# Performance work log

Measured on AMD Instinct MI355X. Metric: run time of the kernel, lower is better.

Reference implementation:

```python
import jax, jax.numpy as jnp
import numpy as np
import math

B, S, D, H, V = 2, 2048, 512, 4, 32000
WINDOWS = [None, 128, 512, None]  # per-head attention windows (None = unlimited)


def setup_inputs() -> dict:
    key = jax.random.key(0)
    ks = jax.random.split(key, 8)
    input_ids = jax.random.randint(ks[0], (B, S), 0, V, dtype=jnp.int64)
    padding_mask = jnp.zeros((B, S), dtype=bool)  # True = pad
    embed_table = jax.random.normal(ks[1], (V, D), dtype=jnp.float32) * 0.02
    self_factors = jnp.full((H,), 0.1, dtype=jnp.float32)
    distance_alphas = jnp.full((H,), 0.1, dtype=jnp.float32)
    # torch Linear weights: [out_features, in_features], xavier-uniform init
    lim_f = math.sqrt(6.0 / (H * D + D))
    fusion_w = jax.random.uniform(ks[2], (D, H * D), jnp.float32, -lim_f, lim_f)
    fusion_b = jnp.zeros((D,), jnp.float32)
    lim_o = math.sqrt(6.0 / (D + V))
    out_w = jax.random.uniform(ks[3], (V, D), jnp.float32, -lim_o, lim_o)
    out_b = jnp.zeros((V,), jnp.float32)
    return {
        "input_ids": input_ids,
        "padding_mask": padding_mask,
        "embed_table": embed_table,
        "self_factors": self_factors,
        "distance_alphas": distance_alphas,
        "fusion_w": fusion_w,
        "fusion_b": fusion_b,
        "out_w": out_w,
        "out_b": out_b,
    }


def reference(input_ids, padding_mask, embed_table, self_factors,
              distance_alphas, fusion_w, fusion_b, out_w, out_b):
    b, s = input_ids.shape
    d = embed_table.shape[1]
    h = self_factors.shape[0]

    emb = embed_table[input_ids]  # [B,S,D]

    pos = jnp.arange(s)
    dist = jnp.abs(pos[:, None] - pos[None, :])          # [S,S]
    causal = pos[None, :] > pos[:, None]                  # [S,S] strict upper triangle
    eye = dist == 0                                       # [S,S]

    # shared raw scores, computed once (same for all heads)
    base = jnp.einsum('bqd,bkd->bqk', emb, emb) / math.sqrt(d)  # [B,S,S]

    # per-head distance decay bias: [H,S,S]
    decay = 1.0 / (1.0 + distance_alphas[:, None, None] * dist.astype(jnp.float32))

    scores = base[None, :, :, :] * decay[:, None, :, :]   # [H,B,S,S]
    # diagonal self-factor scaling
    scores = jnp.where(eye[None, None],
                       scores * self_factors[:, None, None, None], scores)

    # per-head window mask (None -> window >= S, never masks)
    win = jnp.array([s if w is None else w for w in WINDOWS[:h]])
    window_mask = dist[None, :, :] > win[:, None, None]   # [H,S,S]

    # key padding mask, diagonal exempted (as in original)
    key_pad = padding_mask[:, None, :] & (~eye[None])      # [B,S,S]

    full_mask = (window_mask[:, None] | causal[None, None] | key_pad[None])  # [H,B,S,S]
    scores = jnp.where(full_mask, -jnp.inf, scores)

    attn = jax.nn.softmax(scores, axis=-1)                 # [H,B,S,S]
    ctx = jnp.einsum('hbqk,bkd->hbqd', attn, emb)          # [H,B,S,D]

    concat = jnp.moveaxis(ctx, 0, 2).reshape(b, s, h * d)  # [B,S,H*D]
    fused = concat @ fusion_w.T + fusion_b                 # [B,S,D]
    logits = fused @ out_w.T + out_b                       # [B,S,V]
    return logits
```

## Files before the change

### kernel.cpp

```cpp
#include <hip/hip_runtime.h>
#include <hip/hip_bf16.h>
#include <stdint.h>

#define BB 2
#define SB 2048
#define DD 512
#define HH 4
#define VV 32000

typedef __attribute__((ext_vector_type(4))) float f32x4;
typedef __attribute__((ext_vector_type(8))) short bf16x8;
typedef __attribute__((ext_vector_type(4))) unsigned short us4;

__device__ __forceinline__ unsigned short f2bf(float f) {
    unsigned u = __float_as_uint(f);
    u += 0x7fffu + ((u >> 16) & 1u);
    return (unsigned short)(u >> 16);
}

__device__ __forceinline__ __attribute__((address_space(3))) unsigned int*
as_lds(void* p) {
    return (__attribute__((address_space(3))) unsigned int*)(unsigned)(uintptr_t)p;
}
__device__ __forceinline__ const __attribute__((address_space(1))) unsigned int*
as_gbl(const void* p) {
    return (const __attribute__((address_space(1))) unsigned int*)(uintptr_t)p;
}

__global__ void k_cvt_bf16(const float* __restrict__ src, unsigned short* __restrict__ dst, int n) {
    int idx = (blockIdx.x * blockDim.x + threadIdx.x) * 4;
    int stride = gridDim.x * blockDim.x * 4;
    for (int i = idx; i < n; i += stride) {
        float4 v = *(const float4*)(src + i);
        us4 o;
        o.x = f2bf(v.x); o.y = f2bf(v.y); o.z = f2bf(v.z); o.w = f2bf(v.w);
        *(us4*)(dst + i) = o;
    }
}

__global__ void k_embed(const int* __restrict__ ids, const float* __restrict__ tbl,
                        unsigned short* __restrict__ emb) {
    int row = blockIdx.x;
    int id = ids[row];
    if (id < 0) id = 0;
    if (id >= VV) id = VV - 1;
    const float* s = tbl + (size_t)id * DD;
    unsigned short* d = emb + (size_t)row * DD;
    int t = threadIdx.x;
    d[t]       = f2bf(s[t]);
    d[t + 256] = f2bf(s[t + 256]);
}

__global__ void k_dtab_lsum(const float* __restrict__ als,
                            float* __restrict__ dtab, float* __restrict__ lsum) {
    int i = blockIdx.x * 256 + threadIdx.x;
    if (i < HH * SB) {
        int h = i >> 11, d = i & (SB - 1);
        dtab[i] = 0.04419417382415922f / (1.f + als[h] * (float)d);
    } else {
        lsum[i - HH * SB] = 0.f;
    }
}

__global__ void k_embT(const unsigned short* __restrict__ emb, unsigned short* __restrict__ embT) {
    const int d0 = blockIdx.x * 64, s0 = blockIdx.y * 64, b = blockIdx.z;
    __shared__ unsigned short TT[64][72];
    const int t = threadIdx.x;
    {
        int s = t >> 2, c16 = (t & 3) * 16;
        const unsigned short* src = emb + ((size_t)(b * SB + s0 + s)) * DD + d0 + c16;
        bf16x8 v0 = *(const bf16x8*)src;
        bf16x8 v1 = *(const bf16x8*)(src + 8);
#pragma unroll
        for (int j = 0; j < 8; ++j) {
            TT[c16 + j][s]     = (unsigned short)v0[j];
            TT[c16 + 8 + j][s] = (unsigned short)v1[j];
        }
    }
    __syncthreads();
    {
        int d = t >> 2, sc = (t & 3) * 16;
        bf16x8 o0, o1;
#pragma unroll
        for (int j = 0; j < 8; ++j) {
            o0[j] = (short)TT[d][sc + j];
            o1[j] = (short)TT[d][sc + 8 + j];
        }
        unsigned short* dst = embT + ((size_t)(b * DD + d0 + d)) * SB + s0 + sc;
        *(bf16x8*)dst = o0;
        *(bf16x8*)(dst + 8) = o1;
    }
}

__launch_bounds__(256, 2)
__global__ void k_base(const unsigned short* __restrict__ emb,
                       const unsigned char* __restrict__ pad,
                       const float* __restrict__ sfs,
                       const float* __restrict__ dtab,
                       unsigned short* __restrict__ P,
                       float* __restrict__ lsum)
{
    const int kt = blockIdx.x, qt = blockIdx.y, b = blockIdx.z;
    if (kt > qt + 1) return;
    const int tid = threadIdx.x, lane = tid & 63, wv = tid >> 6;
    const int l15 = lane & 15, g = lane >> 4;

    if (kt == qt + 1) {
        int row = tid >> 2, cb = (tid & 3) * 16;
        int4 z = {0, 0, 0, 0};
#pragma unroll
        for (int h = 0; h < 4; ++h) {
            unsigned short* Ph = P + (((size_t)(h * 2 + b)) * SB + qt * 64 + row) * SB + kt * 64 + cb;
            *(int4*)Ph = z;
            *(int4*)(Ph + 8) = z;
        }
        return;
    }

    __shared__ __align__(16) unsigned short Ql[64 * 128];
    __shared__ __align__(16) unsigned short Kl[64 * 128];

    const int q = qt * 64 + wv * 16 + l15;

    f32x4 zero4 = {0.f, 0.f, 0.f, 0.f};
    f32x4 cc[4];
#pragma unroll
    for (int c = 0; c < 4; ++c) cc[c] = zero4;

    for (int dc = 0; dc < 4; ++dc) {
        const int d0 = dc * 128;
        __syncthreads();
#pragma unroll
        for (int i = 0; i < 4; ++i) {
            int flat = (i * 256 + tid) * 8;
            int row = flat >> 7;
            int ch  = (flat >> 3) & 15;
            int scol = ((ch ^ (row & 15)) << 3);
            __builtin_amdgcn_global_load_lds(
                as_gbl(emb + ((size_t)(b * SB + qt * 64 + row)) * DD + d0 + scol),
                as_lds(Ql + flat), 16, 0, 0);
            __builtin_amdgcn_global_load_lds(
                as_gbl(emb + ((size_t)(b * SB + kt * 64 + row)) * DD + d0 + scol),
                as_lds(Kl + flat), 16, 0, 0);
        }
        asm volatile("s_waitcnt vmcnt(0)" ::: "memory");
        __syncthreads();

#pragma unroll
        for (int dsl = 0; dsl < 4; ++dsl) {
            int chr = (dsl * 4 + g);
            bf16x8 qf = *(const bf16x8*)(Ql + (wv * 16 + l15) * 128 + ((chr ^ l15) << 3));
#pragma unroll
            for (int c = 0; c < 4; ++c) {
                bf16x8 kf = *(const bf16x8*)(Kl + (c * 16 + l15) * 128 + ((chr ^ l15) << 3));
                cc[c] = __builtin_amdgcn_mfma_f32_16x16x32_bf16(kf, qf, cc[c], 0, 0, 0);
            }
        }
    }

    unsigned long long padm = __ballot(pad[(size_t)b * SB + kt * 64 + lane] != 0);

    const int wins[4] = {1 << 30, 128, 512, 1 << 30};
#pragma unroll
    for (int h = 0; h < 4; ++h) {
        const int win = wins[h];
        if (kt * 64 + win + 192 < qt * 64) continue;
        const float sf = sfs[h];
        const float* dth = dtab + h * SB;
        float rsum = 0.f;
        unsigned short pb[4][4];
#pragma unroll
        for (int c = 0; c < 4; ++c) {
#pragma unroll
            for (int r = 0; r < 4; ++r) {
                int kk = kt * 64 + c * 16 + 4 * g + r;
                int dist = q - kk;
                float p = 0.f;
                if (dist >= 0 && dist <= win &&
                    ((dist == 0) || !((padm >> (c * 16 + 4 * g + r)) & 1ull))) {
                    float s = cc[c][r] * dth[dist];
                    if (dist == 0) s *= sf;
                    p = __expf(s);
                }
                rsum += p;
                pb[c][r] = f2bf(p);
            }
        }
        unsigned short* Ph = P + (((size_t)(h * 2 + b)) * SB + q) * SB + kt * 64;
#pragma unroll
        for (int c = 0; c < 4; ++c) {
            us4 o;
            o.x = pb[c][0]; o.y = pb[c][1]; o.z = pb[c][2]; o.w = pb[c][3];
            *(us4*)(Ph + c * 16 + 4 * g) = o;
        }
        rsum += __shfl_xor(rsum, 16, 64);
        rsum += __shfl_xor(rsum, 32, 64);
        if (lane < 16)
            atomicAdd(&lsum[((size_t)(h * 2 + b)) * SB + q], rsum);
    }
}

__launch_bounds__(256, 2)
__global__ void k_pv(const unsigned short* __restrict__ P,
                     const unsigned short* __restrict__ embT,
                     const float* __restrict__ lsum,
                     unsigned short* __restrict__ concat)
{
    const int t64 = blockIdx.x, b = blockIdx.y, h = blockIdx.z;
    const int mt = t64 >> 2, nt = t64 & 3;
    const int Q0 = mt * 128;
    const int win = (h == 1) ? 128 : (h == 2) ? 512 : (1 << 30);
    int klo = Q0 - win - 64; if (klo < 0) klo = 0; klo &= ~63;
    const int khi = Q0 + 128;

    __shared__ __align__(16) unsigned short Al[128 * 32];
    __shared__ __align__(16) unsigned short Bl[128 * 32];

    const int tid = threadIdx.x, lane = tid & 63, wv = tid >> 6;
    const int wm = (wv >> 1) * 64, wn = (wv & 1) * 64;
    const int l15 = lane & 15, g = lane >> 4;

    f32x4 zero4 = {0.f, 0.f, 0.f, 0.f};
    f32x4 acc[4][4];
#pragma unroll
    for (int i = 0; i < 4; ++i)
#pragma unroll
        for (int j = 0; j < 4; ++j) acc[i][j] = zero4;

    const unsigned short* Ab = P + (((size_t)(h * 2 + b)) * SB + Q0) * SB;
    const unsigned short* Bb = embT + ((size_t)(b * DD + nt * 128)) * SB;

    for (int k0 = klo; k0 < khi; k0 += 32) {
        __syncthreads();
#pragma unroll
        for (int s = 0; s < 2; ++s) {
            int e = (s * 256 + tid) * 8;
            int row = e >> 5, col = e & 31;
            __builtin_amdgcn_global_load_lds(as_gbl(Ab + (size_t)row * SB + k0 + col),
                                             as_lds(Al + e), 16, 0, 0);
            __builtin_amdgcn_global_load_lds(as_gbl(Bb + (size_t)row * SB + k0 + col),
                                             as_lds(Bl + e), 16, 0, 0);
        }
        asm volatile("s_waitcnt vmcnt(0)" ::: "memory");
        __syncthreads();

        bf16x8 af[4], bfr[4];
#pragma unroll
        for (int i = 0; i < 4; ++i) {
            af[i]  = *(const bf16x8*)(Al + (wm + i * 16 + l15) * 32 + 8 * g);
            bfr[i] = *(const bf16x8*)(Bl + (wn + i * 16 + l15) * 32 + 8 * g);
        }
#pragma unroll
        for (int i = 0; i < 4; ++i)
#pragma unroll
            for (int j = 0; j < 4; ++j)
                acc[i][j] = __builtin_amdgcn_mfma_f32_16x16x32_bf16(af[i], bfr[j], acc[i][j], 0, 0, 0);
    }

    const float* ls = lsum + ((size_t)(h * 2 + b)) * SB;
    unsigned short* cb = concat + ((size_t)(b * SB)) * (HH * DD) + h * DD + nt * 128;
#pragma unroll
    for (int i = 0; i < 4; ++i) {
        int rowb = wm + i * 16 + g * 4;
        float inv[4];
#pragma unroll
        for (int rr = 0; rr < 4; ++rr) inv[rr] = 1.f / ls[Q0 + rowb + rr];
#pragma unroll
        for (int j = 0; j < 4; ++j) {
            int col = wn + j * 16 + l15;
#pragma unroll
            for (int rr = 0; rr < 4; ++rr)
                cb[(size_t)(Q0 + rowb + rr) * (HH * DD) + col] = f2bf(acc[i][j][rr] * inv[rr]);
        }
    }
}

template <int OUTF32>
__launch_bounds__(256, 2)
__global__ void k_gemm_bt(const unsigned short* __restrict__ A,
                          const unsigned short* __restrict__ Bt,
                          const float* __restrict__ bias,
                          void* __restrict__ Cout,
                          int M, int N, int K)
{
    const int nMt = M >> 7;
    const int nwg = gridDim.x;
    int bid = blockIdx.x;
    int q = nwg >> 3, r = nwg & 7;
    int x = bid & 7, o = bid >> 3;
    int wg = (x < r ? x * (q + 1) : r * (q + 1) + (x - r) * q) + o;
    const int mt = wg % nMt, nt = wg / nMt;

    __shared__ __align__(16) unsigned short Al[128 * 32];
    __shared__ __align__(16) unsigned short Bl[128 * 32];

    const int tid = threadIdx.x;
    const int lane = tid & 63;
    const int wv = tid >> 6;
    const int wm = (wv >> 1) * 64, wn = (wv & 1) * 64;
    const int l15 = lane & 15, g = lane >> 4;

    f32x4 zero4 = {0.f, 0.f, 0.f, 0.f};
    f32x4 acc[4][4];
#pragma unroll
    for (int i = 0; i < 4; ++i)
#pragma unroll
        for (int j = 0; j < 4; ++j) acc[i][j] = zero4;

    const unsigned short* Ab = A + (size_t)mt * 128 * K;
    const unsigned short* Bb = Bt + (size_t)nt * 128 * K;

    for (int k0 = 0; k0 < K; k0 += 32) {
        __syncthreads();
#pragma unroll
        for (int s = 0; s < 2; ++s) {
            int e = (s * 256 + tid) * 8;
            int row = e >> 5, col = e & 31;
            __builtin_amdgcn_global_load_lds(as_gbl(Ab + (size_t)row * K + k0 + col),
                                             as_lds(Al + e), 16, 0, 0);
            __builtin_amdgcn_global_load_lds(as_gbl(Bb + (size_t)row * K + k0 + col),
                                             as_lds(Bl + e), 16, 0, 0);
        }
        asm volatile("s_waitcnt vmcnt(0)" ::: "memory");
        __syncthreads();

        bf16x8 af[4], bfr[4];
#pragma unroll
        for (int i = 0; i < 4; ++i) {
            af[i]  = *(const bf16x8*)(Al + (wm + i * 16 + l15) * 32 + 8 * g);
            bfr[i] = *(const bf16x8*)(Bl + (wn + i * 16 + l15) * 32 + 8 * g);
        }
#pragma unroll
        for (int i = 0; i < 4; ++i)
#pragma unroll
            for (int j = 0; j < 4; ++j)
                acc[i][j] = __builtin_amdgcn_mfma_f32_16x16x32_bf16(af[i], bfr[j], acc[i][j], 0, 0, 0);
    }

#pragma unroll
    for (int i = 0; i < 4; ++i) {
        int rowb = mt * 128 + wm + i * 16 + g * 4;
#pragma unroll
        for (int j = 0; j < 4; ++j) {
            int col = nt * 128 + wn + j * 16 + l15;
            float bv = bias[col];
            if (OUTF32) {
                float* C = (float*)Cout;
#pragma unroll
                for (int rr = 0; rr < 4; ++rr)
                    C[(size_t)(rowb + rr) * N + col] = acc[i][j][rr] + bv;
            } else {
                unsigned short* C = (unsigned short*)Cout;
#pragma unroll
                for (int rr = 0; rr < 4; ++rr)
                    C[(size_t)(rowb + rr) * N + col] = f2bf(acc[i][j][rr] + bv);
            }
        }
    }
}

extern "C" void kernel_launch(void* const* d_in, const int* in_sizes, int n_in,
                              void* d_out, int out_size, void* d_ws, size_t ws_size,
                              hipStream_t stream)
{
    const int*           ids = (const int*)d_in[0];
    const unsigned char* pad = (const unsigned char*)d_in[1];
    const float*         tbl = (const float*)d_in[2];
    const float*         sfs = (const float*)d_in[3];
    const float*         als = (const float*)d_in[4];
    const float*         fw  = (const float*)d_in[5];
    const float*         fb  = (const float*)d_in[6];
    const float*         ow  = (const float*)d_in[7];
    const float*         ob  = (const float*)d_in[8];
    float* logits = (float*)d_out;

    char* ws = (char*)d_ws;
    unsigned short* outw_bf = (unsigned short*)(ws);
    unsigned short* fusw_bf = (unsigned short*)(ws + 32768000);
    unsigned short* emb_bf  = (unsigned short*)(ws + 34865152);
    unsigned short* concat  = (unsigned short*)(ws + 39059456);
    unsigned short* fused   = (unsigned short*)(ws + 55836672);

    char* ob_scratch = (char*)d_out;
    unsigned short* P    = (unsigned short*)(ob_scratch);
    unsigned short* embT = (unsigned short*)(ob_scratch + 67108864);
    float*          dtab = (float*)(ob_scratch + 71303168);
    float*          lsum = (float*)(ob_scratch + 71335936);

    k_cvt_bf16<<<2048, 256, 0, stream>>>(ow, outw_bf, VV * DD);
    k_cvt_bf16<<<512, 256, 0, stream>>>(fw, fusw_bf, DD * HH * DD);
    k_embed<<<BB * SB, 256, 0, stream>>>(ids, tbl, emb_bf);
    k_dtab_lsum<<<96, 256, 0, stream>>>(als, dtab, lsum);

    dim3 tg(8, 32, BB);
    k_embT<<<tg, 256, 0, stream>>>(emb_bf, embT);

    dim3 bg(32, 32, BB);
    k_base<<<bg, 256, 0, stream>>>(emb_bf, pad, sfs, dtab, P, lsum);

    dim3 pg(64, BB, HH);
    k_pv<<<pg, 256, 0, stream>>>(P, embT, lsum, concat);

    k_gemm_bt<0><<<32 * 4, 256, 0, stream>>>(concat, fusw_bf, fb, fused, BB * SB, DD, HH * DD);
    k_gemm_bt<1><<<32 * 250, 256, 0, stream>>>(fused, outw_bf, ob, logits, BB * SB, VV, DD);
}
```

Baseline: 394.8 us.

## Merge prep kernels into one launch and add 256x256 output-projection GEMM

Folds the four preprocessing kernels (weight bf16 conversion, embedding gather, decay table, transpose) into a single block-indexed launch. The transpose now reads the embedding table directly, so it no longer waits on the bf16 embedding buffer. The large vocab projection switches to a new 512-thread GEMM with 256x256 tiles, a 4-deep global_load_lds pipeline, XOR-swizzled LDS, priority hints and XCD-aware block remapping. This cuts launch overhead and raises data reuse in the dominant GEMM, at the cost of higher LDS use (128KB) and register pressure.

```diff
diff --git a/kernel.cpp b/kernel.cpp
--- a/kernel.cpp
+++ b/kernel.cpp
@@ -27,68 +27,87 @@
     return (const __attribute__((address_space(1))) unsigned int*)(uintptr_t)p;
 }
 
-__global__ void k_cvt_bf16(const float* __restrict__ src, unsigned short* __restrict__ dst, int n) {
-    int idx = (blockIdx.x * blockDim.x + threadIdx.x) * 4;
-    int stride = gridDim.x * blockDim.x * 4;
-    for (int i = idx; i < n; i += stride) {
-        float4 v = *(const float4*)(src + i);
-        us4 o;
-        o.x = f2bf(v.x); o.y = f2bf(v.y); o.z = f2bf(v.z); o.w = f2bf(v.w);
-        *(us4*)(dst + i) = o;
-    }
-}
-
-__global__ void k_embed(const int* __restrict__ ids, const float* __restrict__ tbl,
-                        unsigned short* __restrict__ emb) {
-    int row = blockIdx.x;
-    int id = ids[row];
-    if (id < 0) id = 0;
-    if (id >= VV) id = VV - 1;
-    const float* s = tbl + (size_t)id * DD;
-    unsigned short* d = emb + (size_t)row * DD;
-    int t = threadIdx.x;
-    d[t]       = f2bf(s[t]);
-    d[t + 256] = f2bf(s[t + 256]);
-}
-
-__global__ void k_dtab_lsum(const float* __restrict__ als,
-                            float* __restrict__ dtab, float* __restrict__ lsum) {
-    int i = blockIdx.x * 256 + threadIdx.x;
-    if (i < HH * SB) {
-        int h = i >> 11, d = i & (SB - 1);
-        dtab[i] = 0.04419417382415922f / (1.f + als[h] * (float)d);
+__device__ __forceinline__ bf16x8 ldsrd(const unsigned short* base, int row, int g) {
+    int byte = row * 64 + (((g) ^ (row & 3)) << 4);
+    return *(const bf16x8*)((const char*)base + byte);
+}
+
+__global__ void k_prep(const int* __restrict__ ids, const float* __restrict__ tbl,
+                       const float* __restrict__ als,
+                       const float* __restrict__ fw, const float* __restrict__ ow,
+                       unsigned short* __restrict__ outw_bf, unsigned short* __restrict__ fusw_bf,
+                       unsigned short* __restrict__ emb, unsigned short* __restrict__ embT,
+                       float* __restrict__ dtab, float* __restrict__ lsum)
+{
+    __shared__ unsigned short TT[64][72];
+    const int bid = blockIdx.x, t = threadIdx.x;
+
+    if (bid < 2000) {
+        int base = bid * 8192 + t * 4;
+#pragma unroll
+        for (int it = 0; it < 8; ++it) {
+            int i = base + it * 1024;
+            float4 v = *(const float4*)(ow + i);
+            us4 o; o.x = f2bf(v.x); o.y = f2bf(v.y); o.z = f2bf(v.z); o.w = f2bf(v.w);
+            *(us4*)(outw_bf + i) = o;
+        }
+    } else if (bid < 2256) {
+        int base = (bid - 2000) * 4096 + t * 4;
+#pragma unroll
+        for (int it = 0; it < 4; ++it) {
+            int i = base + it * 1024;
+            float4 v = *(const float4*)(fw + i);
+            us4 o; o.x = f2bf(v.x); o.y = f2bf(v.y); o.z = f2bf(v.z); o.w = f2bf(v.w);
+            *(us4*)(fusw_bf + i) = o;
+        }
+    } else if (bid < 6352) {
+        int row = bid - 2256;
+        int id = ids[row];
+        if (id < 0) id = 0;
+        if (id >= VV) id = VV - 1;
+        const float* s = tbl + (size_t)id * DD;
+        unsigned short* d = emb + (size_t)row * DD;
+        d[t]       = f2bf(s[t]);
+        d[t + 256] = f2bf(s[t + 256]);
+    } else if (bid < 6448) {
+        int i = (bid - 6352) * 256 + t;
+        if (i < HH * SB) {
+            int h = i >> 11, dd = i & (SB - 1);
+            dtab[i] = 0.04419417382415922f / (1.f + als[h] * (float)dd);
+        } else {
+            lsum[i - HH * SB] = 0.f;
+        }
     } else {
-        lsum[i - HH * SB] = 0.f;
-    }
-}
-
-__global__ void k_embT(const unsigned short* __restrict__ emb, unsigned short* __restrict__ embT) {
-    const int d0 = blockIdx.x * 64, s0 = blockIdx.y * 64, b = blockIdx.z;
-    __shared__ unsigned short TT[64][72];
-    const int t = threadIdx.x;
-    {
-        int s = t >> 2, c16 = (t & 3) * 16;
-        const unsigned short* src = emb + ((size_t)(b * SB + s0 + s)) * DD + d0 + c16;
-        bf16x8 v0 = *(const bf16x8*)src;
-        bf16x8 v1 = *(const bf16x8*)(src + 8);
-#pragma unroll
-        for (int j = 0; j < 8; ++j) {
-            TT[c16 + j][s]     = (unsigned short)v0[j];
-            TT[c16 + 8 + j][s] = (unsigned short)v1[j];
-        }
-    }
-    __syncthreads();
-    {
-        int d = t >> 2, sc = (t & 3) * 16;
-        bf16x8 o0, o1;
-#pragma unroll
-        for (int j = 0; j < 8; ++j) {
-            o0[j] = (short)TT[d][sc + j];
-            o1[j] = (short)TT[d][sc + 8 + j];
-        }
-        unsigned short* dst = embT + ((size_t)(b * DD + d0 + d)) * SB + s0 + sc;
-        *(bf16x8*)dst = o0;
-        *(bf16x8*)(dst + 8) = o1;
+        int bid2 = bid - 6448;
+        const int d0 = (bid2 & 7) * 64, s0 = ((bid2 >> 3) & 31) * 64, b = bid2 >> 8;
+        {
+            int s = t >> 2, c16 = (t & 3) * 16;
+            int id = ids[b * SB + s0 + s];
+            if (id < 0) id = 0;
+            if (id >= VV) id = VV - 1;
+            const float* src = tbl + (size_t)id * DD + d0 + c16;
+#pragma unroll
+            for (int q4 = 0; q4 < 4; ++q4) {
+                float4 v = *(const float4*)(src + q4 * 4);
+                TT[c16 + q4 * 4 + 0][s] = f2bf(v.x);
+                TT[c16 + q4 * 4 + 1][s] = f2bf(v.y);
+                TT[c16 + q4 * 4 + 2][s] = f2bf(v.z);
+                TT[c16 + q4 * 4 + 3][s] = f2bf(v.w);
+            }
+        }
+        __syncthreads();
+        {
+            int d = t >> 2, sc = (t & 3) * 16;
+            bf16x8 o0, o1;
+#pragma unroll
+            for (int j = 0; j < 8; ++j) {
+                o0[j] = (short)TT[d][sc + j];
+                o1[j] = (short)TT[d][sc + 8 + j];
+            }
+            unsigned short* dst = embT + ((size_t)(b * DD + d0 + d)) * SB + s0 + sc;
+            *(bf16x8*)dst = o0;
+            *(bf16x8*)(dst + 8) = o1;
+        }
     }
 }
 
@@ -359,6 +378,153 @@
     }
 }
 
+__launch_bounds__(512, 2)
+__global__ void k_gemm256(const unsigned short* __restrict__ A,
+                          const unsigned short* __restrict__ Bt,
+                          const float* __restrict__ bias,
+                          float* __restrict__ Cout,
+                          int M, int N, int K)
+{
+    const int nMt = M >> 8;
+    const int nwg = gridDim.x;
+    int bid = blockIdx.x;
+    int q = nwg >> 3, r = nwg & 7;
+    int x = bid & 7, o = bid >> 3;
+    int wg = (x < r ? x * (q + 1) : r * (q + 1) + (x - r) * q) + o;
+    const int mt = wg % nMt, nt = wg / nMt;
+
+    __shared__ __align__(16) unsigned short Al[4][8192];
+    __shared__ __align__(16) unsigned short Bl[4][8192];
+
+    const int tid = threadIdx.x;
+    const int lane = tid & 63, wv = tid >> 6;
+    const int wr = wv >> 2, wc = wv & 3;
+    const int l15 = lane & 15, g = lane >> 4;
+
+    f32x4 zero4 = {0.f, 0.f, 0.f, 0.f};
+    f32x4 acc[8][4];
+#pragma unroll
+    for (int i = 0; i < 8; ++i)
+#pragma unroll
+        for (int j = 0; j < 4; ++j) acc[i][j] = zero4;
+
+    const unsigned short* Ab = A + (size_t)mt * 256 * K;
+    const unsigned short* Bb = Bt + (size_t)nt * 256 * K;
+
+    const int c0 = tid, c1 = 512 + tid;
+    const int r0 = c0 >> 2, r1 = c1 >> 2;
+    const int sc0 = (((c0 & 3) ^ (r0 & 3)) << 3);
+    const int sc1 = (((c1 & 3) ^ (r1 & 3)) << 3);
+    const unsigned short* Asrc0 = Ab + (size_t)r0 * K + sc0;
+    const unsigned short* Asrc1 = Ab + (size_t)r1 * K + sc1;
+    const unsigned short* Bsrc0 = Bb + (size_t)r0 * K + sc0;
+    const unsigned short* Bsrc1 = Bb + (size_t)r1 * K + sc1;
+
+#define STAGE_A256(rg_, ko_) { \
+    __builtin_amdgcn_global_load_lds(as_gbl(Asrc0 + (ko_)), as_lds(&Al[rg_][c0 * 8]), 16, 0, 0); \
+    __builtin_amdgcn_global_load_lds(as_gbl(Asrc1 + (ko_)), as_lds(&Al[rg_][c1 * 8]), 16, 0, 0); }
+#define STAGE_B256(rg_, ko_) { \
+    __builtin_amdgcn_global_load_lds(as_gbl(Bsrc0 + (ko_)), as_lds(&Bl[rg_][c0 * 8]), 16, 0, 0); \
+    __builtin_amdgcn_global_load_lds(as_gbl(Bsrc1 + (ko_)), as_lds(&Bl[rg_][c1 * 8]), 16, 0, 0); }
+
+#define SBAR { __builtin_amdgcn_sched_barrier(0); __builtin_amdgcn_s_barrier(); __builtin_amdgcn_sched_barrier(0); }
+
+#define GEMM_GROUP(t_, DOSTAGE_, WAIT_)                                          \
+  {                                                                              \
+    const int rg = (t_) & 3;                                                     \
+    const unsigned short* Ar = Al[rg];                                           \
+    const unsigned short* Br = Bl[rg];                                           \
+    bf16x8 bfr0 = ldsrd(Br, wc * 64 +  0 + l15, g);                              \
+    bf16x8 bfr1 = ldsrd(Br, wc * 64 + 16 + l15, g);                              \
+    bf16x8 bfr2 = ldsrd(Br, wc * 64 + 32 + l15, g);                              \
+    bf16x8 bfr3 = ldsrd(Br, wc * 64 + 48 + l15, g);                              \
+    bf16x8 af0 = ldsrd(Ar, wr * 128 +  0 + l15, g);                              \
+    bf16x8 af1 = ldsrd(Ar, wr * 128 + 16 + l15, g);                              \
+    bf16x8 af2 = ldsrd(Ar, wr * 128 + 32 + l15, g);                              \
+    bf16x8 af3 = ldsrd(Ar, wr * 128 + 48 + l15, g);                              \
+    if (DOSTAGE_) STAGE_A256(((t_) + 3) & 3, ((t_) + 3) * 32);                   \
+    SBAR;                                                                        \
+    __builtin_amdgcn_s_setprio(1);                                               \
+    acc[0][0] = __builtin_amdgcn_mfma_f32_16x16x32_bf16(af0, bfr0, acc[0][0], 0, 0, 0); \
+    acc[0][1] = __builtin_amdgcn_mfma_f32_16x16x32_bf16(af0, bfr1, acc[0][1], 0, 0, 0); \
+    acc[0][2] = __builtin_amdgcn_mfma_f32_16x16x32_bf16(af0, bfr2, acc[0][2], 0, 0, 0); \
+    acc[0][3] = __builtin_amdgcn_mfma_f32_16x16x32_bf16(af0, bfr3, acc[0][3], 0, 0, 0); \
+    acc[1][0] = __builtin_amdgcn_mfma_f32_16x16x32_bf16(af1, bfr0, acc[1][0], 0, 0, 0); \
+    acc[1][1] = __builtin_amdgcn_mfma_f32_16x16x32_bf16(af1, bfr1, acc[1][1], 0, 0, 0); \
+    acc[1][2] = __builtin_amdgcn_mfma_f32_16x16x32_bf16(af1, bfr2, acc[1][2], 0, 0, 0); \
+    acc[1][3] = __builtin_amdgcn_mfma_f32_16x16x32_bf16(af1, bfr3, acc[1][3], 0, 0, 0); \
+    acc[2][0] = __builtin_amdgcn_mfma_f32_16x16x32_bf16(af2, bfr0, acc[2][0], 0, 0, 0); \
+    acc[2][1] = __builtin_amdgcn_mfma_f32_16x16x32_bf16(af2, bfr1, acc[2][1], 0, 0, 0); \
+    acc[2][2] = __builtin_amdgcn_mfma_f32_16x16x32_bf16(af2, bfr2, acc[2][2], 0, 0, 0); \
+    acc[2][3] = __builtin_amdgcn_mfma_f32_16x16x32_bf16(af2, bfr3, acc[2][3], 0, 0, 0); \
+    acc[3][0] = __builtin_amdgcn_mfma_f32_16x16x32_bf16(af3, bfr0, acc[3][0], 0, 0, 0); \
+    acc[3][1] = __builtin_amdgcn_mfma_f32_16x16x32_bf16(af3, bfr1, acc[3][1], 0, 0, 0); \
+    acc[3][2] = __builtin_amdgcn_mfma_f32_16x16x32_bf16(af3, bfr2, acc[3][2], 0, 0, 0); \
+    acc[3][3] = __builtin_amdgcn_mfma_f32_16x16x32_bf16(af3, bfr3, acc[3][3], 0, 0, 0); \
+    __builtin_amdgcn_s_setprio(0);                                               \
+    SBAR;                                                                        \
+    bf16x8 ag0 = ldsrd(Ar, wr * 128 +  64 + l15, g);                             \
+    bf16x8 ag1 = ldsrd(Ar, wr * 128 +  80 + l15, g);                             \
+    bf16x8 ag2 = ldsrd(Ar, wr * 128 +  96 + l15, g);                             \
+    bf16x8 ag3 = ldsrd(Ar, wr * 128 + 112 + l15, g);                             \
+    if (DOSTAGE_) STAGE_B256(((t_) + 3) & 3, ((t_) + 3) * 32);                   \
+    WAIT_;                                                                       \
+    SBAR;                                                                        \
+    __builtin_amdgcn_s_setprio(1);                                               \
+    acc[4][0] = __builtin_amdgcn_mfma_f32_16x16x32_bf16(ag0, bfr0, acc[4][0], 0, 0, 0); \
+    acc[4][1] = __builtin_amdgcn_mfma_f32_16x16x32_bf16(ag0, bfr1, acc[4][1], 0, 0, 0); \
+    acc[4][2] = __builtin_amdgcn_mfma_f32_16x16x32_bf16(ag0, bfr2, acc[4][2], 0, 0, 0); \
+    acc[4][3] = __builtin_amdgcn_mfma_f32_16x16x32_bf16(ag0, bfr3, acc[4][3], 0, 0, 0); \
+    acc[5][0] = __builtin_amdgcn_mfma_f32_16x16x32_bf16(ag1, bfr0, acc[5][0], 0, 0, 0); \
+    acc[5][1] = __builtin_amdgcn_mfma_f32_16x16x32_bf16(ag1, bfr1, acc[5][1], 0, 0, 0); \
+    acc[5][2] = __builtin_amdgcn_mfma_f32_16x16x32_bf16(ag1, bfr2, acc[5][2], 0, 0, 0); \
+    acc[5][3] = __builtin_amdgcn_mfma_f32_16x16x32_bf16(ag1, bfr3, acc[5][3], 0, 0, 0); \
+    acc[6][0] = __builtin_amdgcn_mfma_f32_16x16x32_bf16(ag2, bfr0, acc[6][0], 0, 0, 0); \
+    acc[6][1] = __builtin_amdgcn_mfma_f32_16x16x32_bf16(ag2, bfr1, acc[6][1], 0, 0, 0); \
+    acc[6][2] = __builtin_amdgcn_mfma_f32_16x16x32_bf16(ag2, bfr2, acc[6][2], 0, 0, 0); \
+    acc[6][3] = __builtin_amdgcn_mfma_f32_16x16x32_bf16(ag2, bfr3, acc[6][3], 0, 0, 0); \
+    acc[7][0] = __builtin_amdgcn_mfma_f32_16x16x32_bf16(ag3, bfr0, acc[7][0], 0, 0, 0); \
+    acc[7][1] = __builtin_amdgcn_mfma_f32_16x16x32_bf16(ag3, bfr1, acc[7][1], 0, 0, 0); \
+    acc[7][2] = __builtin_amdgcn_mfma_f32_16x16x32_bf16(ag3, bfr2, acc[7][2], 0, 0, 0); \
+    acc[7][3] = __builtin_amdgcn_mfma_f32_16x16x32_bf16(ag3, bfr3, acc[7][3], 0, 0, 0); \
+    __builtin_amdgcn_s_setprio(0);                                               \
+    SBAR;                                                                        \
+  }
+
+    const int NT = K >> 5;
+    STAGE_A256(0, 0);  STAGE_B256(0, 0);
+    STAGE_A256(1, 32); STAGE_B256(1, 32);
+    STAGE_A256(2, 64); STAGE_B256(2, 64);
+    asm volatile("s_waitcnt vmcnt(8)" ::: "memory");
+    SBAR;
+
+    for (int t = 0; t < NT - 3; ++t) {
+        GEMM_GROUP(t, 1, asm volatile("s_waitcnt vmcnt(8)" ::: "memory"));
+    }
+    GEMM_GROUP(NT - 3, 0, asm volatile("s_waitcnt vmcnt(4)" ::: "memory"));
+    GEMM_GROUP(NT - 2, 0, asm volatile("s_waitcnt vmcnt(0)" ::: "memory"));
+    GEMM_GROUP(NT - 1, 0, );
+
+    const int mrow = mt * 256 + wr * 128;
+    const int ncol = nt * 256 + wc * 64;
+#pragma unroll
+    for (int i = 0; i < 8; ++i) {
+        int rowb = mrow + i * 16 + g * 4;
+#pragma unroll
+        for (int j = 0; j < 4; ++j) {
+            int col = ncol + j * 16 + l15;
+            float bv = bias[col];
+#pragma unroll
+            for (int rr = 0; rr < 4; ++rr)
+                Cout[(size_t)(rowb + rr) * N + col] = acc[i][j][rr] + bv;
+        }
+    }
+#undef GEMM_GROUP
+#undef STAGE_A256
+#undef STAGE_B256
+#undef SBAR
+}
+
 extern "C" void kernel_launch(void* const* d_in, const int* in_sizes, int n_in,
                               void* d_out, int out_size, void* d_ws, size_t ws_size,
                               hipStream_t stream)
@@ -387,13 +553,8 @@
     float*          dtab = (float*)(ob_scratch + 71303168);
     float*          lsum = (float*)(ob_scratch + 71335936);
 
-    k_cvt_bf16<<<2048, 256, 0, stream>>>(ow, outw_bf, VV * DD);
-    k_cvt_bf16<<<512, 256, 0, stream>>>(fw, fusw_bf, DD * HH * DD);
-    k_embed<<<BB * SB, 256, 0, stream>>>(ids, tbl, emb_bf);
-    k_dtab_lsum<<<96, 256, 0, stream>>>(als, dtab, lsum);
-
-    dim3 tg(8, 32, BB);
-    k_embT<<<tg, 256, 0, stream>>>(emb_bf, embT);
+    k_prep<<<6960, 256, 0, stream>>>(ids, tbl, als, fw, ow,
+                                     outw_bf, fusw_bf, emb_bf, embT, dtab, lsum);
 
     dim3 bg(32, 32, BB);
     k_base<<<bg, 256, 0, stream>>>(emb_bf, pad, sfs, dtab, P, lsum);
@@ -402,5 +563,5 @@
     k_pv<<<pg, 256, 0, stream>>>(P, embT, lsum, concat);
 
     k_gemm_bt<0><<<32 * 4, 256, 0, stream>>>(concat, fusw_bf, fb, fused, BB * SB, DD, HH * DD);
-    k_gemm_bt<1><<<32 * 250, 256, 0, stream>>>(fused, outw_bf, ob, logits, BB * SB, VV, DD);
-}
+    k_gemm256<<<16 * 125, 512, 0, stream>>>(fused, outw_bf, ob, logits, BB * SB, VV, DD);
+}
```

Result: faster. 386.5 us (-2.1%).
